# Kernel tuning notes

Measured on AMD Instinct MI355X. Metric: run time of the kernel, lower is better.

The kernel has to match this reference:

```python
import jax, jax.numpy as jnp
import numpy as np

EMB = 1024
HEADS = 16
HEAD_DIM = EMB // HEADS


def setup_inputs() -> dict:
    key = jax.random.key(0)
    ks = jax.random.split(key, 12)
    B, S = 4, 2048
    scale = 1.0 / np.sqrt(EMB)
    inp = {
        'values': jax.random.normal(ks[0], (B, S, EMB), jnp.float32),
        'keys': jax.random.normal(ks[1], (B, S, EMB), jnp.float32),
        'query': jax.random.normal(ks[2], (B, S, EMB), jnp.float32),
        'Wv': jax.random.normal(ks[3], (EMB, EMB), jnp.float32) * scale,
        'bv': jnp.zeros((EMB,), jnp.float32),
        'Wk': jax.random.normal(ks[4], (EMB, EMB), jnp.float32) * scale,
        'bk': jnp.zeros((EMB,), jnp.float32),
        'Wq': jax.random.normal(ks[5], (EMB, EMB), jnp.float32) * scale,
        'bq': jnp.zeros((EMB,), jnp.float32),
        'Wo': jax.random.normal(ks[6], (EMB, EMB), jnp.float32) * scale,
        'bo': jnp.zeros((EMB,), jnp.float32),
    }
    return inp


def reference(values, keys, query, Wv, bv, Wk, bk, Wq, bq, Wo, bo):
    B, S, _ = values.shape
    # Linear projections (torch Linear: x @ W.T + b)
    v = values @ Wv.T + bv
    k = keys @ Wk.T + bk
    q = query @ Wq.T + bq
    # Reshape to (B, S, H, D) -- NOTE: original does NOT transpose heads,
    # so attention is computed across the HEAD axis per position.
    v = v.reshape(B, S, HEADS, HEAD_DIM)
    k = k.reshape(B, S, HEADS, HEAD_DIM)
    q = q.reshape(B, S, HEADS, HEAD_DIM)
    # (B,S,H,D) @ (B,S,D,H) -> (B,S,H,H) head-head scores
    scores = jnp.einsum('bshd,bsgd->bshg', q, k) * (HEAD_DIM ** -0.5)
    attn = jax.nn.softmax(scores, axis=-1)
    # (B,S,H,H) @ (B,S,H,D) -> (B,S,H,D)
    out = jnp.einsum('bshg,bsgd->bshd', attn, v)
    out = out.reshape(B, S, EMB)
    return out @ Wo.T + bo
```

## Files before the change

kernel.cpp:

```cpp
#include <hip/hip_runtime.h>
#include <stdint.h>

#define EMB 1024
#define LROW 40

typedef unsigned short u16;
typedef __attribute__((ext_vector_type(8))) unsigned short u16x8;
typedef __attribute__((ext_vector_type(8))) __bf16 bf16x8;
typedef __attribute__((ext_vector_type(4))) float f32x4;

__device__ __forceinline__ u16 f2bf(float f) {
  union { float f; uint32_t u; } x; x.f = f;
  uint32_t u = x.u;
  u += 0x7fff + ((u >> 16) & 1u);
  return (u16)(u >> 16);
}

__device__ __forceinline__ bf16x8 cvt8(float4 a, float4 b) {
  bf16x8 r;
  r[0] = (__bf16)a.x; r[1] = (__bf16)a.y; r[2] = (__bf16)a.z; r[3] = (__bf16)a.w;
  r[4] = (__bf16)b.x; r[5] = (__bf16)b.y; r[6] = (__bf16)b.z; r[7] = (__bf16)b.w;
  return r;
}

__device__ __forceinline__ void gl16(const u16* g, u16* l) {
  __builtin_amdgcn_global_load_lds(
      (const __attribute__((address_space(1))) void*)g,
      (__attribute__((address_space(3))) void*)l, 16, 0, 0);
}

__device__ __forceinline__ int xcd_logical(int orig, int nwg) {
  return (orig & 7) * (nwg >> 3) + (orig >> 3);
}

__global__ __launch_bounds__(256) void cvtw_kernel(
    const float* __restrict__ s0, u16* __restrict__ d0,
    const float* __restrict__ s1, u16* __restrict__ d1,
    const float* __restrict__ s2, u16* __restrict__ d2,
    const float* __restrict__ s3, u16* __restrict__ d3)
{
  const float* s; u16* d;
  switch (blockIdx.y) {
    case 0:  s = s0; d = d0; break;
    case 1:  s = s1; d = d1; break;
    case 2:  s = s2; d = d2; break;
    default: s = s3; d = d3; break;
  }
  const size_t i = (size_t)blockIdx.x * 256 + threadIdx.x;
  const float4* f = (const float4*)(s + i * 8);
  const float4 lo = f[0], hi = f[1];
  *(bf16x8*)(d + i * 8) = cvt8(lo, hi);
}

__global__ __launch_bounds__(256, 3) void qkv_fused_kernel(
    const float* __restrict__ Vx, const float* __restrict__ Kx,
    const float* __restrict__ Qx, const u16* __restrict__ Wb,
    const float* __restrict__ Bv, const float* __restrict__ Bk,
    const float* __restrict__ Bq,
    u16* __restrict__ cv, u16* __restrict__ ck, u16* __restrict__ cq,
    int N, int K, int M)
{
  __shared__ __attribute__((aligned(16))) u16 Al[128 * 32];
  __shared__ __attribute__((aligned(16))) u16 Bl[128 * 32];

  const int nwg = (N >> 7) * (M >> 7) * 3;
  const int logical = xcd_logical(blockIdx.x, nwg);
  const int per_z = (N >> 7) * (M >> 7);
  const int z = logical / per_z;
  const int rem = logical - z * per_z;
  const int nbx = N >> 7;
  const int by = rem / nbx, bx = rem - by * nbx;

  const float* X; const u16* W; const float* Bias; u16* C;
  switch (z) {
    case 0:  X = Vx; W = Wb;                   Bias = Bv; C = cv; break;
    case 1:  X = Kx; W = Wb + EMB * EMB;       Bias = Bk; C = ck; break;
    default: X = Qx; W = Wb + 2 * EMB * EMB;   Bias = Bq; C = cq; break;
  }

  const int tid  = threadIdx.x;
  const int lane = tid & 63;
  const int w    = tid >> 6;
  const int wm = w >> 1, wn = w & 1;
  const int r16 = lane & 15, quad = lane >> 4;
  const int bm = by * 128, bn = bx * 128;

  const int s0 = tid, s1 = tid + 256;
  const int r0 = s0 >> 2, c0 = s0 & 3;
  const int r1 = s1 >> 2, c1 = s1 & 3;
  const int lA0 = r0 * 32 + ((c0 ^ ((r0 >> 1) & 3)) * 8);
  const int lA1 = r1 * 32 + ((c1 ^ ((r1 >> 1) & 3)) * 8);
  const size_t xo0 = (size_t)(bm + r0) * K + c0 * 8;
  const size_t xo1 = (size_t)(bm + r1) * K + c1 * 8;

  const int bs0 = w * 64 + lane, bs1 = bs0 + 256;
  const int br0 = bs0 >> 2, bc0 = ((bs0 & 3) ^ ((br0 >> 1) & 3)) * 8;
  const int br1 = bs1 >> 2, bc1 = ((bs1 & 3) ^ ((br1 >> 1) & 3)) * 8;
  const u16* srcB0 = W + (size_t)(bn + br0) * K + bc0;
  const u16* srcB1 = W + (size_t)(bn + br1) * K + bc1;
  u16* dB0 = Bl + (w * 64) * 8;
  u16* dB1 = dB0 + 256 * 8;

  const int swz = (quad ^ ((r16 >> 1) & 3)) * 8;
  int offA[4], offB[4];
#pragma unroll
  for (int t = 0; t < 4; t++) {
    offA[t] = (wm * 64 + t * 16 + r16) * 32 + swz;
    offB[t] = (wn * 64 + t * 16 + r16) * 32 + swz;
  }

  f32x4 acc[4][4];
#pragma unroll
  for (int i = 0; i < 4; i++)
#pragma unroll
    for (int j = 0; j < 4; j++)
      acc[i][j] = f32x4{0.f, 0.f, 0.f, 0.f};

  float4 xa0 = *(const float4*)(X + xo0), xa1 = *(const float4*)(X + xo0 + 4);
  float4 xb0 = *(const float4*)(X + xo1), xb1 = *(const float4*)(X + xo1 + 4);

  for (int k0 = 0; k0 < K; k0 += 32) {
    *(bf16x8*)&Al[lA0] = cvt8(xa0, xa1);
    *(bf16x8*)&Al[lA1] = cvt8(xb0, xb1);
    gl16(srcB0 + k0, dB0);
    gl16(srcB1 + k0, dB1);
    __syncthreads();

    const int kn = (k0 + 32 < K) ? (k0 + 32) : 0;
    xa0 = *(const float4*)(X + xo0 + kn); xa1 = *(const float4*)(X + xo0 + kn + 4);
    xb0 = *(const float4*)(X + xo1 + kn); xb1 = *(const float4*)(X + xo1 + kn + 4);

    bf16x8 a[4], b[4];
#pragma unroll
    for (int t = 0; t < 4; t++) a[t] = *(const bf16x8*)&Al[offA[t]];
#pragma unroll
    for (int t = 0; t < 4; t++) b[t] = *(const bf16x8*)&Bl[offB[t]];

#pragma unroll
    for (int tm = 0; tm < 4; tm++)
#pragma unroll
      for (int tn = 0; tn < 4; tn++)
        acc[tm][tn] = __builtin_amdgcn_mfma_f32_16x16x32_bf16(a[tm], b[tn], acc[tm][tn], 0, 0, 0);
    __syncthreads();
  }

#pragma unroll
  for (int tn = 0; tn < 4; tn++) {
    const int col = bn + wn * 64 + tn * 16 + r16;
    const float bias = Bias[col];
#pragma unroll
    for (int tm = 0; tm < 4; tm++) {
      const int row0 = bm + wm * 64 + tm * 16 + quad * 4;
#pragma unroll
      for (int r = 0; r < 4; r++)
        C[(size_t)(row0 + r) * N + col] = f2bf(acc[tm][tn][r] + bias);
    }
  }
}

__global__ __launch_bounds__(256, 3) void out_gemm_kernel(
    const u16* __restrict__ X, const u16* __restrict__ W,
    const float* __restrict__ Bias, float* __restrict__ C, int N, int K, int M)
{
  __shared__ __attribute__((aligned(16))) u16 Al[128 * 32];
  __shared__ __attribute__((aligned(16))) u16 Bl[128 * 32];

  const int nwg = (N >> 7) * (M >> 7);
  const int logical = xcd_logical(blockIdx.x, nwg);
  const int nbx = N >> 7;
  const int by = logical / nbx, bx = logical - by * nbx;

  const int tid  = threadIdx.x;
  const int lane = tid & 63;
  const int w    = tid >> 6;
  const int wm = w >> 1, wn = w & 1;
  const int r16 = lane & 15, quad = lane >> 4;
  const int bm = by * 128, bn = bx * 128;

  const int s0 = w * 64 + lane, s1 = s0 + 256;
  const int r0 = s0 >> 2, c0 = ((s0 & 3) ^ ((r0 >> 1) & 3)) * 8;
  const int r1 = s1 >> 2, c1 = ((s1 & 3) ^ ((r1 >> 1) & 3)) * 8;

  const u16* srcA0 = X + (size_t)(bm + r0) * K + c0;
  const u16* srcA1 = X + (size_t)(bm + r1) * K + c1;
  const u16* srcB0 = W + (size_t)(bn + r0) * K + c0;
  const u16* srcB1 = W + (size_t)(bn + r1) * K + c1;

  u16* dA0 = Al + (w * 64) * 8;
  u16* dA1 = dA0 + 256 * 8;
  u16* dB0 = Bl + (w * 64) * 8;
  u16* dB1 = dB0 + 256 * 8;

  const int swz = (quad ^ ((r16 >> 1) & 3)) * 8;
  int offA[4], offB[4];
#pragma unroll
  for (int t = 0; t < 4; t++) {
    offA[t] = (wm * 64 + t * 16 + r16) * 32 + swz;
    offB[t] = (wn * 64 + t * 16 + r16) * 32 + swz;
  }

  f32x4 acc[4][4];
#pragma unroll
  for (int i = 0; i < 4; i++)
#pragma unroll
    for (int j = 0; j < 4; j++)
      acc[i][j] = f32x4{0.f, 0.f, 0.f, 0.f};

  for (int k0 = 0; k0 < K; k0 += 32) {
    gl16(srcA0 + k0, dA0);
    gl16(srcA1 + k0, dA1);
    gl16(srcB0 + k0, dB0);
    gl16(srcB1 + k0, dB1);
    __syncthreads();

    bf16x8 a[4], b[4];
#pragma unroll
    for (int t = 0; t < 4; t++) a[t] = *(const bf16x8*)&Al[offA[t]];
#pragma unroll
    for (int t = 0; t < 4; t++) b[t] = *(const bf16x8*)&Bl[offB[t]];

#pragma unroll
    for (int tm = 0; tm < 4; tm++)
#pragma unroll
      for (int tn = 0; tn < 4; tn++)
        acc[tm][tn] = __builtin_amdgcn_mfma_f32_16x16x32_bf16(a[tm], b[tn], acc[tm][tn], 0, 0, 0);
    __syncthreads();
  }

#pragma unroll
  for (int tn = 0; tn < 4; tn++) {
    const int col = bn + wn * 64 + tn * 16 + r16;
    const float bias = Bias[col];
#pragma unroll
    for (int tm = 0; tm < 4; tm++) {
      const int row0 = bm + wm * 64 + tm * 16 + quad * 4;
#pragma unroll
      for (int r = 0; r < 4; r++)
        C[(size_t)(row0 + r) * N + col] = acc[tm][tn][r] + bias;
    }
  }
}

__global__ __launch_bounds__(256, 4) void attn_heads_kernel(
    const u16* Q, const u16* Km, const u16* V, u16* O)
{
  __shared__ __attribute__((aligned(16))) u16 P[4][16 * LROW];
  __shared__ __attribute__((aligned(16))) u16 VT[4][64 * LROW];

  const int tid = threadIdx.x, lane = tid & 63, w = tid >> 6;
  const int r16 = lane & 15, quad = lane >> 4;
  const size_t base = ((size_t)blockIdx.x * 4 + w) * EMB;

  const bf16x8 aq0 = *(const bf16x8*)&Q[base + r16 * 64 + quad * 8];
  const bf16x8 aq1 = *(const bf16x8*)&Q[base + r16 * 64 + 32 + quad * 8];
  const bf16x8 bk0 = *(const bf16x8*)&Km[base + r16 * 64 + quad * 8];
  const bf16x8 bk1 = *(const bf16x8*)&Km[base + r16 * 64 + 32 + quad * 8];

  const u16x8 v0 = *(const u16x8*)&V[base + lane * 16];
  const u16x8 v1 = *(const u16x8*)&V[base + lane * 16 + 8];
  const u16x8 z8 = {0, 0, 0, 0, 0, 0, 0, 0};
  *(u16x8*)&VT[w][lane * LROW + 16] = z8;
  *(u16x8*)&VT[w][lane * LROW + 24] = z8;
  const int g = lane >> 2, dbase = (lane & 3) * 16;
#pragma unroll
  for (int i = 0; i < 8; i++) {
    VT[w][(dbase + i) * LROW + g]     = v0[i];
    VT[w][(dbase + 8 + i) * LROW + g] = v1[i];
  }

  f32x4 s = f32x4{0.f, 0.f, 0.f, 0.f};
  s = __builtin_amdgcn_mfma_f32_16x16x32_bf16(aq0, bk0, s, 0, 0, 0);
  s = __builtin_amdgcn_mfma_f32_16x16x32_bf16(aq1, bk1, s, 0, 0, 0);

  float p[4];
#pragma unroll
  for (int r = 0; r < 4; r++) {
    float v = s[r] * 0.125f;
    float m = v;
#pragma unroll
    for (int d = 8; d; d >>= 1) m = fmaxf(m, __shfl_xor(m, d, 16));
    float e = __expf(v - m);
    float sum = e;
#pragma unroll
    for (int d = 8; d; d >>= 1) sum += __shfl_xor(sum, d, 16);
    p[r] = e / sum;
  }

#pragma unroll
  for (int r = 0; r < 4; r++) {
    P[w][(quad * 4 + r) * LROW + r16]      = f2bf(p[r]);
    P[w][(quad * 4 + r) * LROW + 16 + r16] = 0;
  }
  __syncthreads();

  const bf16x8 pa = *(const bf16x8*)&P[w][r16 * LROW + quad * 8];

#pragma unroll
  for (int c = 0; c < 4; c++) {
    const bf16x8 bvv = *(const bf16x8*)&VT[w][(c * 16 + r16) * LROW + quad * 8];
    f32x4 o = f32x4{0.f, 0.f, 0.f, 0.f};
    o = __builtin_amdgcn_mfma_f32_16x16x32_bf16(pa, bvv, o, 0, 0, 0);
#pragma unroll
    for (int r = 0; r < 4; r++)
      O[base + (size_t)(quad * 4 + r) * 64 + c * 16 + r16] = f2bf(o[r]);
  }
}

extern "C" void kernel_launch(void* const* d_in, const int* in_sizes, int n_in,
                              void* d_out, int out_size, void* d_ws, size_t ws_size,
                              hipStream_t stream)
{
  const float* values = (const float*)d_in[0];
  const float* keys   = (const float*)d_in[1];
  const float* query  = (const float*)d_in[2];
  const float* Wv = (const float*)d_in[3];
  const float* bv = (const float*)d_in[4];
  const float* Wk = (const float*)d_in[5];
  const float* bk = (const float*)d_in[6];
  const float* Wq = (const float*)d_in[7];
  const float* bq = (const float*)d_in[8];
  const float* Wo = (const float*)d_in[9];
  const float* bo = (const float*)d_in[10];

  const int M = in_sizes[0] / EMB;
  const int N = EMB, K = EMB;

  u16* q    = (u16*)d_ws;
  u16* kbuf = q + (size_t)M * EMB;
  u16* v    = (u16*)d_out;
  u16* wb   = v + (size_t)M * EMB;
  u16* ao   = q;

  const size_t base_ws = (size_t)2 * M * EMB * sizeof(u16);
  const bool wo_in_ws = ws_size >= base_ws + (size_t)EMB * EMB * sizeof(u16);
  u16* wob = wo_in_ws ? kbuf + (size_t)M * EMB : kbuf;

  dim3 blk(256, 1, 1);
  dim3 cwg(EMB * EMB / 8 / 256, wo_in_ws ? 4 : 3, 1);

  hipLaunchKernelGGL(cvtw_kernel, cwg, blk, 0, stream,
                     Wv, wb, Wk, wb + EMB * EMB, Wq, wb + 2 * EMB * EMB, Wo, wob);
  hipLaunchKernelGGL(qkv_fused_kernel, dim3((N / 128) * (M / 128) * 3, 1, 1), blk, 0, stream,
                     values, keys, query, wb, bv, bk, bq, v, kbuf, q, N, K, M);
  hipLaunchKernelGGL(attn_heads_kernel, dim3(M / 4, 1, 1), blk, 0, stream,
                     q, kbuf, v, ao);
  if (!wo_in_ws)
    hipLaunchKernelGGL(cvtw_kernel, dim3(EMB * EMB / 8 / 256, 1, 1), blk, 0, stream,
                       Wo, wob, (const float*)nullptr, (u16*)nullptr,
                       (const float*)nullptr, (u16*)nullptr,
                       (const float*)nullptr, (u16*)nullptr);
  hipLaunchKernelGGL(out_gemm_kernel, dim3((N / 128) * (M / 128), 1, 1), blk, 0, stream,
                     ao, wob, bo, (float*)d_out, N, K, M);
}
```

Before: 282.3 us.

## Double-buffer LDS tiles in QKV and output GEMMs with single barrier per step

Measured after the change: 282.7 us. About the same (+0.2%).

```diff
diff --git a/kernel.cpp b/kernel.cpp
--- a/kernel.cpp
+++ b/kernel.cpp
@@ -60,8 +60,8 @@
     u16* __restrict__ cv, u16* __restrict__ ck, u16* __restrict__ cq,
     int N, int K, int M)
 {
-  __shared__ __attribute__((aligned(16))) u16 Al[128 * 32];
-  __shared__ __attribute__((aligned(16))) u16 Bl[128 * 32];
+  __shared__ __attribute__((aligned(16))) u16 Al[2][128 * 32];
+  __shared__ __attribute__((aligned(16))) u16 Bl[2][128 * 32];
 
   const int nwg = (N >> 7) * (M >> 7) * 3;
   const int logical = xcd_logical(blockIdx.x, nwg);
@@ -98,8 +98,7 @@
   const int br1 = bs1 >> 2, bc1 = ((bs1 & 3) ^ ((br1 >> 1) & 3)) * 8;
   const u16* srcB0 = W + (size_t)(bn + br0) * K + bc0;
   const u16* srcB1 = W + (size_t)(bn + br1) * K + bc1;
-  u16* dB0 = Bl + (w * 64) * 8;
-  u16* dB1 = dB0 + 256 * 8;
+  const int dB0o = (w * 64) * 8, dB1o = dB0o + 256 * 8;
 
   const int swz = (quad ^ ((r16 >> 1) & 3)) * 8;
   int offA[4], offB[4];
@@ -118,30 +117,43 @@
 
   float4 xa0 = *(const float4*)(X + xo0), xa1 = *(const float4*)(X + xo0 + 4);
   float4 xb0 = *(const float4*)(X + xo1), xb1 = *(const float4*)(X + xo1 + 4);
+  *(bf16x8*)&Al[0][lA0] = cvt8(xa0, xa1);
+  *(bf16x8*)&Al[0][lA1] = cvt8(xb0, xb1);
+  gl16(srcB0, &Bl[0][dB0o]);
+  gl16(srcB1, &Bl[0][dB1o]);
+  __builtin_amdgcn_sched_barrier(0);
+  xa0 = *(const float4*)(X + xo0 + 32); xa1 = *(const float4*)(X + xo0 + 36);
+  xb0 = *(const float4*)(X + xo1 + 32); xb1 = *(const float4*)(X + xo1 + 36);
+  asm volatile("s_waitcnt vmcnt(4) lgkmcnt(0)\n\ts_barrier" ::: "memory");
 
   for (int k0 = 0; k0 < K; k0 += 32) {
-    *(bf16x8*)&Al[lA0] = cvt8(xa0, xa1);
-    *(bf16x8*)&Al[lA1] = cvt8(xb0, xb1);
-    gl16(srcB0 + k0, dB0);
-    gl16(srcB1 + k0, dB1);
-    __syncthreads();
-
-    const int kn = (k0 + 32 < K) ? (k0 + 32) : 0;
-    xa0 = *(const float4*)(X + xo0 + kn); xa1 = *(const float4*)(X + xo0 + kn + 4);
-    xb0 = *(const float4*)(X + xo1 + kn); xb1 = *(const float4*)(X + xo1 + kn + 4);
+    const int cur = (k0 >> 5) & 1, nxt = cur ^ 1;
+    const int kn  = (k0 + 32) & (K - 1);
+    const int kn2 = (k0 + 64) & (K - 1);
+
+    *(bf16x8*)&Al[nxt][lA0] = cvt8(xa0, xa1);
+    *(bf16x8*)&Al[nxt][lA1] = cvt8(xb0, xb1);
+    gl16(srcB0 + kn, &Bl[nxt][dB0o]);
+    gl16(srcB1 + kn, &Bl[nxt][dB1o]);
+    __builtin_amdgcn_sched_barrier(0);
+    xa0 = *(const float4*)(X + xo0 + kn2); xa1 = *(const float4*)(X + xo0 + kn2 + 4);
+    xb0 = *(const float4*)(X + xo1 + kn2); xb1 = *(const float4*)(X + xo1 + kn2 + 4);
 
     bf16x8 a[4], b[4];
 #pragma unroll
-    for (int t = 0; t < 4; t++) a[t] = *(const bf16x8*)&Al[offA[t]];
-#pragma unroll
-    for (int t = 0; t < 4; t++) b[t] = *(const bf16x8*)&Bl[offB[t]];
+    for (int t = 0; t < 4; t++) a[t] = *(const bf16x8*)&Al[cur][offA[t]];
+#pragma unroll
+    for (int t = 0; t < 4; t++) b[t] = *(const bf16x8*)&Bl[cur][offB[t]];
+    asm volatile("s_waitcnt lgkmcnt(0)" ::: "memory");
+    __builtin_amdgcn_sched_barrier(0);
 
 #pragma unroll
     for (int tm = 0; tm < 4; tm++)
 #pragma unroll
       for (int tn = 0; tn < 4; tn++)
         acc[tm][tn] = __builtin_amdgcn_mfma_f32_16x16x32_bf16(a[tm], b[tn], acc[tm][tn], 0, 0, 0);
-    __syncthreads();
+
+    asm volatile("s_waitcnt vmcnt(4)\n\ts_barrier" ::: "memory");
   }
 
 #pragma unroll
@@ -162,8 +174,8 @@
     const u16* __restrict__ X, const u16* __restrict__ W,
     const float* __restrict__ Bias, float* __restrict__ C, int N, int K, int M)
 {
-  __shared__ __attribute__((aligned(16))) u16 Al[128 * 32];
-  __shared__ __attribute__((aligned(16))) u16 Bl[128 * 32];
+  __shared__ __attribute__((aligned(16))) u16 Al[2][128 * 32];
+  __shared__ __attribute__((aligned(16))) u16 Bl[2][128 * 32];
 
   const int nwg = (N >> 7) * (M >> 7);
   const int logical = xcd_logical(blockIdx.x, nwg);
@@ -186,10 +198,7 @@
   const u16* srcB0 = W + (size_t)(bn + r0) * K + c0;
   const u16* srcB1 = W + (size_t)(bn + r1) * K + c1;
 
-  u16* dA0 = Al + (w * 64) * 8;
-  u16* dA1 = dA0 + 256 * 8;
-  u16* dB0 = Bl + (w * 64) * 8;
-  u16* dB1 = dB0 + 256 * 8;
+  const int dA0o = (w * 64) * 8, dA1o = dA0o + 256 * 8;
 
   const int swz = (quad ^ ((r16 >> 1) & 3)) * 8;
   int offA[4], offB[4];
@@ -206,25 +215,36 @@
     for (int j = 0; j < 4; j++)
       acc[i][j] = f32x4{0.f, 0.f, 0.f, 0.f};
 
+  gl16(srcA0, &Al[0][dA0o]);
+  gl16(srcA1, &Al[0][dA1o]);
+  gl16(srcB0, &Bl[0][dA0o]);
+  gl16(srcB1, &Bl[0][dA1o]);
+  asm volatile("s_waitcnt vmcnt(0)\n\ts_barrier" ::: "memory");
+
   for (int k0 = 0; k0 < K; k0 += 32) {
-    gl16(srcA0 + k0, dA0);
-    gl16(srcA1 + k0, dA1);
-    gl16(srcB0 + k0, dB0);
-    gl16(srcB1 + k0, dB1);
-    __syncthreads();
+    const int cur = (k0 >> 5) & 1, nxt = cur ^ 1;
+    const int kn = (k0 + 32) & (K - 1);
+
+    gl16(srcA0 + kn, &Al[nxt][dA0o]);
+    gl16(srcA1 + kn, &Al[nxt][dA1o]);
+    gl16(srcB0 + kn, &Bl[nxt][dA0o]);
+    gl16(srcB1 + kn, &Bl[nxt][dA1o]);
 
     bf16x8 a[4], b[4];
 #pragma unroll
-    for (int t = 0; t < 4; t++) a[t] = *(const bf16x8*)&Al[offA[t]];
-#pragma unroll
-    for (int t = 0; t < 4; t++) b[t] = *(const bf16x8*)&Bl[offB[t]];
+    for (int t = 0; t < 4; t++) a[t] = *(const bf16x8*)&Al[cur][offA[t]];
+#pragma unroll
+    for (int t = 0; t < 4; t++) b[t] = *(const bf16x8*)&Bl[cur][offB[t]];
+    asm volatile("s_waitcnt lgkmcnt(0)" ::: "memory");
+    __builtin_amdgcn_sched_barrier(0);
 
 #pragma unroll
     for (int tm = 0; tm < 4; tm++)
 #pragma unroll
       for (int tn = 0; tn < 4; tn++)
         acc[tm][tn] = __builtin_amdgcn_mfma_f32_16x16x32_bf16(a[tm], b[tn], acc[tm][tn], 0, 0, 0);
-    __syncthreads();
+
+    asm volatile("s_waitcnt vmcnt(0)\n\ts_barrier" ::: "memory");
   }
 
 #pragma unroll
```
